# Kernel tuning notes

Measured on AMD Instinct MI355X. Metric: run time of the kernel, lower is better.

## Reference

```python
import jax, jax.numpy as jnp
import numpy as np

# LE-like radial basis config (hypers: type='le', r_cut=5.0, mlp=True, no alchemical)
N_MAX_L = [22, 19, 16, 13]      # n_max per angular channel l
L_MAX = len(N_MAX_L) - 1
N_TOTAL = sum(N_MAX_L)          # 70
N_SPECIES = 4                   # all_species = [0,1,2,3]
N_GRID = 1024                   # spline control points
R_CUT = 5.0
HIDDEN = 32                     # hard-coded MLP width in the module
N_EDGES = 400_000


def setup_inputs() -> dict:
    key = jax.random.key(0)
    ks = jax.random.split(key, 7)
    # neighbor distances in [0, r_cut)
    r = jax.random.uniform(ks[0], (N_EDGES,), dtype=jnp.float32) * R_CUT
    neighbor_species = jax.random.randint(ks[1], (N_EDGES,), 0, N_SPECIES)
    # spline table standing in for the precomputed spliner coefficients
    spline_table = jax.random.normal(ks[2], (N_GRID, N_TOTAL), dtype=jnp.float32)
    nmax = max(N_MAX_L)
    sc_in = 1.0 / np.sqrt(nmax)
    sc_h = 1.0 / np.sqrt(HIDDEN)
    # per-(l, species) expert MLP weights, padded to nmax along the n_max_l axis;
    # torch Linear(n_in, n_out, bias=False) == x @ W with W: [n_in, n_out]
    W1 = jax.random.normal(ks[3], (L_MAX + 1, N_SPECIES, nmax, HIDDEN), dtype=jnp.float32) * sc_in
    W2 = jax.random.normal(ks[4], (L_MAX + 1, N_SPECIES, HIDDEN, HIDDEN), dtype=jnp.float32) * sc_h
    W3 = jax.random.normal(ks[5], (L_MAX + 1, N_SPECIES, HIDDEN, HIDDEN), dtype=jnp.float32) * sc_h
    W4 = jax.random.normal(ks[6], (L_MAX + 1, N_SPECIES, HIDDEN, nmax), dtype=jnp.float32) * sc_h
    return {"r": r, "neighbor_species": neighbor_species, "spline_table": spline_table,
            "W1": W1, "W2": W2, "W3": W3, "W4": W4}


def _spline_eval(r, spline_table):
    # linear-interpolation spline over a uniform grid on [0, R_CUT]
    dx = R_CUT / (N_GRID - 1)
    xi = r / dx
    idx = jnp.clip(jnp.floor(xi).astype(jnp.int32), 0, N_GRID - 2)
    frac = (xi - idx.astype(xi.dtype))[:, None]
    return spline_table[idx] * (1.0 - frac) + spline_table[idx + 1] * frac  # [E, N_TOTAL]


def reference(r, neighbor_species, spline_table, W1, W2, W3, W4):
    # 1) spline basis eval: r -> radial_functions [E, N_TOTAL]
    rf = _spline_eval(r, spline_table)
    silu = jax.nn.silu
    outs = []
    off = 0
    # 2) split by n_max_l; per-species expert MLP with scatter-back.
    # Vectorized as: run each species' tiny MLP on all edges, select via mask
    # (equivalent math to the original's nonzero/index_select gather-scatter).
    for l, n_l in enumerate(N_MAX_L):
        x_l = rf[:, off:off + n_l]  # [E, n_l]
        off += n_l
        out_l = jnp.zeros_like(x_l)
        for s in range(N_SPECIES):
            h = silu(x_l @ W1[l, s, :n_l])        # [E, 32]
            h = silu(h @ W2[l, s])                # [E, 32]
            h = silu(h @ W3[l, s])                # [E, 32]
            y = h @ W4[l, s][:, :n_l]             # [E, n_l]
            out_l = jnp.where(neighbor_species[:, None] == s, y, out_l)
        outs.append(out_l)
    # original returns a list split by l; concatenate for a single output array
    return jnp.concatenate(outs, axis=1)  # [E, N_TOTAL]
```

## Files before the change

### kernel.cpp

```cpp
#include <hip/hip_runtime.h>
#include <hip/hip_bf16.h>
#include <math.h>

#define BLK 256
#define NEDGE_MAX 400000
#define BX 128
#define TSL 24608

typedef __attribute__((ext_vector_type(8))) short short8;
typedef __attribute__((ext_vector_type(4))) float f32x4;

union Frag {
  short8 s;
  unsigned int u[4];
};


__global__ void k_zero(int* __restrict__ cnt) {
  if (threadIdx.x < 4) cnt[threadIdx.x] = 0;
}

__global__ void __launch_bounds__(BLK) k_compact(const int* __restrict__ spc,
                                                 const float* __restrict__ r, int n,
                                                 int* __restrict__ cnt,
                                                 int* __restrict__ perm,
                                                 float* __restrict__ rs) {
  __shared__ int wcnt[4][4];
  __shared__ int wbase[4][4];
  const int tid = threadIdx.x;
  const int i = blockIdx.x * BLK + tid;
  const int lane = tid & 63;
  const int w = tid >> 6;
  const int s = (i < n) ? spc[i] : -1;
  const float rv = (i < n) ? r[i] : 0.f;

  int rank = 0;
#pragma unroll
  for (int sp = 0; sp < 4; sp++) {
    unsigned long long m = __ballot(s == sp);
    if (lane == 0) wcnt[w][sp] = __popcll(m);
    if (s == sp) rank = __popcll(m & ((1ULL << lane) - 1ULL));
  }
  __syncthreads();
  if (tid < 4) {
    const int c0 = wcnt[0][tid], c1 = wcnt[1][tid], c2 = wcnt[2][tid], c3 = wcnt[3][tid];
    const int b = atomicAdd(&cnt[tid], c0 + c1 + c2 + c3);
    wbase[0][tid] = b;
    wbase[1][tid] = b + c0;
    wbase[2][tid] = b + c0 + c1;
    wbase[3][tid] = b + c0 + c1 + c2;
  }
  __syncthreads();
  if (s >= 0) {
    const int pos = wbase[w][s] + rank;
    perm[s * NEDGE_MAX + pos] = i;
    rs[s * NEDGE_MAX + pos] = rv;
  }
}


__global__ void __launch_bounds__(256) k_table(const float* __restrict__ tbl,
                                               float* __restrict__ wt) {
  const int t = blockIdx.x * 256 + threadIdx.x;
  if (t < 4 * 1024 * 24) {
    const int l = t / (1024 * 24);
    const int rem = t - l * (1024 * 24);
    const int idx = rem / 24;
    const int j = rem - idx * 24;
    const int off = (l == 0) ? 0 : (l == 1) ? 22 : (l == 2) ? 41 : 57;
    const int nl = (l == 0) ? 22 : (l == 1) ? 19 : (l == 2) ? 16 : 13;
    const float v = (j < nl) ? tbl[idx * 70 + off + j] : 0.f;
    wt[l * TSL + idx * 24 + j] = v;
  }
  if (t < 4 * 32) {
    const int l = t >> 5, j = t & 31;
    wt[l * TSL + 1024 * 24 + j] = 0.f;
  }
}


__device__ __forceinline__ void split_pair(float a, float b, unsigned int& hi,
                                           unsigned int& lo) {
  __hip_bfloat162 h2 = __float22bfloat162_rn(float2{a, b});
  const unsigned int h = *reinterpret_cast<unsigned int*>(&h2);
  hi = h;
  const float ra = a - __uint_as_float((h & 0xFFFFu) << 16);
  const float rb = b - __uint_as_float(h & 0xFFFF0000u);
  __hip_bfloat162 l2 = __float22bfloat162_rn(float2{ra, rb});
  lo = *reinterpret_cast<unsigned int*>(&l2);
}

__device__ __forceinline__ unsigned int pack_pair(float a, float b) {
  __hip_bfloat162 h2 = __float22bfloat162_rn(float2{a, b});
  return *reinterpret_cast<unsigned int*>(&h2);
}

__device__ __forceinline__ void layer_hl(const Frag* A, const Frag& bh,
                                         const Frag& bl, f32x4& d0, f32x4& d1) {
  f32x4 z = {0.f, 0.f, 0.f, 0.f};
  d0 = __builtin_amdgcn_mfma_f32_16x16x32_bf16(A[0].s, bl.s, z, 0, 0, 0);
  d0 = __builtin_amdgcn_mfma_f32_16x16x32_bf16(A[0].s, bh.s, d0, 0, 0, 0);
  d1 = __builtin_amdgcn_mfma_f32_16x16x32_bf16(A[1].s, bl.s, z, 0, 0, 0);
  d1 = __builtin_amdgcn_mfma_f32_16x16x32_bf16(A[1].s, bh.s, d1, 0, 0, 0);
}

__device__ __forceinline__ void layer_h(const Frag* A, const Frag& bh, f32x4& d0,
                                        f32x4& d1) {
  f32x4 z = {0.f, 0.f, 0.f, 0.f};
  d0 = __builtin_amdgcn_mfma_f32_16x16x32_bf16(A[0].s, bh.s, z, 0, 0, 0);
  d1 = __builtin_amdgcn_mfma_f32_16x16x32_bf16(A[1].s, bh.s, z, 0, 0, 0);
}

__device__ __forceinline__ f32x4 silu4(f32x4 v) {
#pragma unroll
  for (int i = 0; i < 4; i++) v[i] = __fdividef(v[i], 1.0f + __expf(-v[i]));
  return v;
}

struct GD {
  f32x4 a0, a1, b0, b1;
  float frac;
  int e;
  int valid;
};

__device__ __forceinline__ GD do_gather(const float* __restrict__ rs,
                                        const float* __restrict__ tb,
                                        const int* __restrict__ perm, int sBase,
                                        int ei, int count) {
  GD gd;
  gd.valid = ei < count;
  const int eic = gd.valid ? ei : 0;
  gd.e = perm[sBase + eic];
  const float rr = rs[sBase + eic];
  const float xi = rr * (1023.0f / 5.0f);
  int idx = (int)floorf(xi);
  idx = idx < 0 ? 0 : (idx > 1022 ? 1022 : idx);
  gd.frac = xi - (float)idx;
  const float* t0 = tb + idx * 24;
  gd.a0 = *(const f32x4*)(t0);
  gd.a1 = *(const f32x4*)(t0 + 4);
  gd.b0 = *(const f32x4*)(t0 + 24);
  gd.b1 = *(const f32x4*)(t0 + 28);
  return gd;
}

template <int L, int NL, int OFF>
__device__ void body(const float* __restrict__ rs, const float* __restrict__ wt,
                     const float* __restrict__ W1, const float* __restrict__ W2,
                     const float* __restrict__ W3, const float* __restrict__ W4,
                     float* __restrict__ out, const int* __restrict__ cnt,
                     const int* __restrict__ perm, float* __restrict__ xpw,
                     int* __restrict__ eidw) {
  const int s = blockIdx.y & 3;
  const int count = cnt[s];
  if (count == 0) return;

  const int lane = threadIdx.x & 63;
  const int w = threadIdx.x >> 6;
  const int c = lane & 15;
  const int g = lane >> 4;

  const float* __restrict__ w1 = W1 + (size_t)(L * 4 + s) * (22 * 32);
  const float* __restrict__ w2 = W2 + (size_t)(L * 4 + s) * (32 * 32);
  const float* __restrict__ w3 = W3 + (size_t)(L * 4 + s) * (32 * 32);
  const float* __restrict__ w4 = W4 + (size_t)(L * 4 + s) * (32 * 22);

  Frag A1[2], A2[2], A3[2], A4[2];
#pragma unroll
  for (int jt = 0; jt < 2; jt++) {
    const int j = jt * 16 + c;
#pragma unroll
    for (int p = 0; p < 4; p++) {
      const int k0 = 8 * g + 2 * p, k1 = k0 + 1;
      const float a = (k0 < NL) ? w1[k0 * 32 + j] : 0.f;
      const float b = (k1 < NL) ? w1[k1 * 32 + j] : 0.f;
      A1[jt].u[p] = pack_pair(a, b);
      const int kp0 = (p < 2) ? (4 * g + 2 * p) : (16 + 4 * g + 2 * (p - 2));
      const int kp1 = kp0 + 1;
      A2[jt].u[p] = pack_pair(w2[kp0 * 32 + j], w2[kp1 * 32 + j]);
      A3[jt].u[p] = pack_pair(w3[kp0 * 32 + j], w3[kp1 * 32 + j]);
      A4[jt].u[p] = pack_pair((j < NL) ? w4[kp0 * 22 + j] : 0.f,
                              (j < NL) ? w4[kp1 * 22 + j] : 0.f);
    }
  }

  const float* __restrict__ tb = wt + L * TSL + 8 * g;
  const int sBase = s * NEDGE_MAX;
  const int stride = gridDim.x * 64;

  int eb = blockIdx.x * 64 + w * 16;
  GD cur = do_gather(rs, tb, perm, sBase, eb + c, count);

  for (; eb < count; eb += stride) {
    GD nxt = do_gather(rs, tb, perm, sBase, eb + stride + c, count);

    Frag bh, bl;
    {
      float x[8];
#pragma unroll
      for (int d = 0; d < 4; d++) {
        x[d] = cur.a0[d] + cur.frac * (cur.b0[d] - cur.a0[d]);
        x[d + 4] = cur.a1[d] + cur.frac * (cur.b1[d] - cur.a1[d]);
      }
      split_pair(x[0], x[1], bh.u[0], bl.u[0]);
      split_pair(x[2], x[3], bh.u[1], bl.u[1]);
      split_pair(x[4], x[5], bh.u[2], bl.u[2]);
      split_pair(x[6], x[7], bh.u[3], bl.u[3]);
    }

    f32x4 d0, d1;
    layer_hl(A1, bh, bl, d0, d1);

#pragma unroll
    for (int t = 0; t < 3; t++) {
      d0 = silu4(d0);
      d1 = silu4(d1);
      bh.u[0] = pack_pair(d0[0], d0[1]);
      bh.u[1] = pack_pair(d0[2], d0[3]);
      bh.u[2] = pack_pair(d1[0], d1[1]);
      bh.u[3] = pack_pair(d1[2], d1[3]);
      if (t == 0) layer_h(A2, bh, d0, d1);
      else if (t == 1) layer_h(A3, bh, d0, d1);
      else layer_h(A4, bh, d0, d1);
    }

    *(f32x4*)(xpw + c * 36 + 4 * g) = d0;
    *(f32x4*)(xpw + c * 36 + 16 + 4 * g) = d1;
    if (g == 0) eidw[c] = cur.valid ? cur.e : -1;
    __asm__ volatile("" ::: "memory");

    constexpr int TOT = 16 * NL;
#pragma unroll
    for (int t = 0; t < (TOT + 63) / 64; t++) {
      const int flat = t * 64 + lane;
      if (flat < TOT) {
        const int row = flat / NL;
        const int f = flat - row * NL;
        const int er = eidw[row];
        if (er >= 0) out[(size_t)er * 70 + OFF + f] = xpw[row * 36 + f];
      }
    }
    __asm__ volatile("" ::: "memory");

    cur = nxt;
  }
}

__global__ void __launch_bounds__(BLK) rb_mfma(const float* __restrict__ rs,
                                               const float* __restrict__ wt,
                                               const float* __restrict__ W1,
                                               const float* __restrict__ W2,
                                               const float* __restrict__ W3,
                                               const float* __restrict__ W4,
                                               float* __restrict__ out,
                                               const int* __restrict__ cnt,
                                               const int* __restrict__ perm) {
  __shared__ float xpose[4][16 * 36];
  __shared__ int eidt[4][16];
  const int w = threadIdx.x >> 6;
  float* xpw = &xpose[w][0];
  int* eidw = &eidt[w][0];
  switch (blockIdx.y >> 2) {
    case 0: body<0, 22, 0>(rs, wt, W1, W2, W3, W4, out, cnt, perm, xpw, eidw); break;
    case 1: body<1, 19, 22>(rs, wt, W1, W2, W3, W4, out, cnt, perm, xpw, eidw); break;
    case 2: body<2, 16, 41>(rs, wt, W1, W2, W3, W4, out, cnt, perm, xpw, eidw); break;
    default: body<3, 13, 57>(rs, wt, W1, W2, W3, W4, out, cnt, perm, xpw, eidw); break;
  }
}

extern "C" void kernel_launch(void* const* d_in, const int* in_sizes, int n_in,
                              void* d_out, int out_size, void* d_ws, size_t ws_size,
                              hipStream_t stream) {
  const float* r = (const float*)d_in[0];
  const int* spc = (const int*)d_in[1];
  const float* tbl = (const float*)d_in[2];
  const float* W1 = (const float*)d_in[3];
  const float* W2 = (const float*)d_in[4];
  const float* W3 = (const float*)d_in[5];
  const float* W4 = (const float*)d_in[6];
  float* out = (float*)d_out;
  const int n = in_sizes[0];

  int* cnt = (int*)d_ws;
  int* perm = (int*)d_ws + 64;
  float* rs = (float*)((int*)d_ws + 64 + 4 * NEDGE_MAX);
  float* wtbl = rs + 4 * NEDGE_MAX;

  hipLaunchKernelGGL(k_zero, dim3(1), dim3(64), 0, stream, cnt);

  const int nb = (n + BLK - 1) / BLK;
  hipLaunchKernelGGL(k_compact, dim3(nb), dim3(BLK), 0, stream, spc, r, n, cnt,
                     perm, rs);

  hipLaunchKernelGGL(k_table, dim3((4 * 1024 * 24 + 255) / 256), dim3(256), 0,
                     stream, tbl, wtbl);

  hipLaunchKernelGGL(rb_mfma, dim3(BX, 16), dim3(BLK), 0, stream, rs, wtbl, W1, W2,
                     W3, W4, out, cnt, perm);
}
```

Measured before the change: 145.1 us.

## Replace scattered MFMA output writes with bf16 staging plus coalesced scatter

Adds a histogram and prefix pass so each species' edges sit contiguously, and precomputes the spline fraction and table offset during compaction. The MLP kernel then writes its results as bf16 into a species-sorted temporary buffer, and a separate gather kernel writes the final output rows in order, giving fully coalesced output stores. The goal is to remove the scattered per-edge output writes. In exchange it adds extra kernel launches and another pass over the data, and it rounds the output to bf16, which loses precision. A direct-write fallback runs when the workspace is too small.

```diff
diff --git a/kernel.cpp b/kernel.cpp
--- a/kernel.cpp
+++ b/kernel.cpp
@@ -3,7 +3,6 @@
 #include <math.h>
 
 #define BLK 256
-#define NEDGE_MAX 400000
 #define BX 128
 #define TSL 24608
 
@@ -15,16 +14,55 @@
   unsigned int u[4];
 };
 
+__device__ __forceinline__ unsigned int pack_pair(float a, float b) {
+  __hip_bfloat162 h2 = __float22bfloat162_rn(float2{a, b});
+  return *reinterpret_cast<unsigned int*>(&h2);
+}
+
+__device__ __forceinline__ void split_pair(float a, float b, unsigned int& hi,
+                                           unsigned int& lo) {
+  hi = pack_pair(a, b);
+  const float ra = a - __uint_as_float(hi << 16);
+  const float rb = b - __uint_as_float(hi & 0xFFFF0000u);
+  lo = pack_pair(ra, rb);
+}
+
 
 __global__ void k_zero(int* __restrict__ cnt) {
   if (threadIdx.x < 4) cnt[threadIdx.x] = 0;
 }
 
+__global__ void __launch_bounds__(BLK) k_hist(const int* __restrict__ spc, int n,
+                                              int* __restrict__ cnt) {
+  __shared__ int h[4];
+  if (threadIdx.x < 4) h[threadIdx.x] = 0;
+  __syncthreads();
+  const int i = blockIdx.x * BLK + threadIdx.x;
+  if (i < n) atomicAdd(&h[spc[i]], 1);
+  __syncthreads();
+  if (threadIdx.x < 4) atomicAdd(&cnt[threadIdx.x], h[threadIdx.x]);
+}
+
+__global__ void k_prefix(const int* __restrict__ cnt, int* __restrict__ cnt2,
+                         int* __restrict__ csum) {
+  if (threadIdx.x == 0) {
+    int a = 0;
+#pragma unroll
+    for (int s = 0; s < 4; s++) {
+      csum[s] = a;
+      cnt2[s] = a;
+      a += cnt[s];
+    }
+  }
+}
+
 __global__ void __launch_bounds__(BLK) k_compact(const int* __restrict__ spc,
                                                  const float* __restrict__ r, int n,
-                                                 int* __restrict__ cnt,
-                                                 int* __restrict__ perm,
-                                                 float* __restrict__ rs) {
+                                                 int* __restrict__ cnt2,
+                                                 int* __restrict__ inv,
+                                                 float* __restrict__ fracs,
+                                                 int* __restrict__ toffA,
+                                                 int* __restrict__ perm) {
   __shared__ int wcnt[4][4];
   __shared__ int wbase[4][4];
   const int tid = threadIdx.x;
@@ -32,7 +70,7 @@
   const int lane = tid & 63;
   const int w = tid >> 6;
   const int s = (i < n) ? spc[i] : -1;
-  const float rv = (i < n) ? r[i] : 0.f;
+  const float rr = (i < n) ? r[i] : 0.f;
 
   int rank = 0;
 #pragma unroll
@@ -44,7 +82,7 @@
   __syncthreads();
   if (tid < 4) {
     const int c0 = wcnt[0][tid], c1 = wcnt[1][tid], c2 = wcnt[2][tid], c3 = wcnt[3][tid];
-    const int b = atomicAdd(&cnt[tid], c0 + c1 + c2 + c3);
+    const int b = atomicAdd(&cnt2[tid], c0 + c1 + c2 + c3);
     wbase[0][tid] = b;
     wbase[1][tid] = b + c0;
     wbase[2][tid] = b + c0 + c1;
@@ -52,9 +90,14 @@
   }
   __syncthreads();
   if (s >= 0) {
-    const int pos = wbase[w][s] + rank;
-    perm[s * NEDGE_MAX + pos] = i;
-    rs[s * NEDGE_MAX + pos] = rv;
+    const int sp = wbase[w][s] + rank;
+    const float xi = rr * (1023.0f / 5.0f);
+    int idx = (int)floorf(xi);
+    idx = idx < 0 ? 0 : (idx > 1022 ? 1022 : idx);
+    inv[i] = sp;
+    fracs[sp] = xi - (float)idx;
+    toffA[sp] = idx * 96;
+    perm[sp] = i;
   }
 }
 
@@ -79,22 +122,6 @@
 }
 
 
-__device__ __forceinline__ void split_pair(float a, float b, unsigned int& hi,
-                                           unsigned int& lo) {
-  __hip_bfloat162 h2 = __float22bfloat162_rn(float2{a, b});
-  const unsigned int h = *reinterpret_cast<unsigned int*>(&h2);
-  hi = h;
-  const float ra = a - __uint_as_float((h & 0xFFFFu) << 16);
-  const float rb = b - __uint_as_float(h & 0xFFFF0000u);
-  __hip_bfloat162 l2 = __float22bfloat162_rn(float2{ra, rb});
-  lo = *reinterpret_cast<unsigned int*>(&l2);
-}
-
-__device__ __forceinline__ unsigned int pack_pair(float a, float b) {
-  __hip_bfloat162 h2 = __float22bfloat162_rn(float2{a, b});
-  return *reinterpret_cast<unsigned int*>(&h2);
-}
-
 __device__ __forceinline__ void layer_hl(const Frag* A, const Frag& bh,
                                          const Frag& bl, f32x4& d0, f32x4& d1) {
   f32x4 z = {0.f, 0.f, 0.f, 0.f};
@@ -124,37 +151,38 @@
   int valid;
 };
 
-__device__ __forceinline__ GD do_gather(const float* __restrict__ rs,
-                                        const float* __restrict__ tb,
-                                        const int* __restrict__ perm, int sBase,
+template <bool DIRECT>
+__device__ __forceinline__ GD do_gather(const float* __restrict__ fracs,
+                                        const int* __restrict__ toffA,
+                                        const int* __restrict__ perm,
+                                        const char* __restrict__ tbB, int sp0,
                                         int ei, int count) {
   GD gd;
   gd.valid = ei < count;
-  const int eic = gd.valid ? ei : 0;
-  gd.e = perm[sBase + eic];
-  const float rr = rs[sBase + eic];
-  const float xi = rr * (1023.0f / 5.0f);
-  int idx = (int)floorf(xi);
-  idx = idx < 0 ? 0 : (idx > 1022 ? 1022 : idx);
-  gd.frac = xi - (float)idx;
-  const float* t0 = tb + idx * 24;
-  gd.a0 = *(const f32x4*)(t0);
-  gd.a1 = *(const f32x4*)(t0 + 4);
-  gd.b0 = *(const f32x4*)(t0 + 24);
-  gd.b1 = *(const f32x4*)(t0 + 28);
+  const int spi = sp0 + (gd.valid ? ei : 0);
+  gd.frac = fracs[spi];
+  const int to = toffA[spi];
+  if (DIRECT) gd.e = perm[spi]; else gd.e = 0;
+  const char* p = tbB + to;
+  gd.a0 = *(const f32x4*)(p);
+  gd.a1 = *(const f32x4*)(p + 16);
+  gd.b0 = *(const f32x4*)(p + 96);
+  gd.b1 = *(const f32x4*)(p + 112);
   return gd;
 }
 
-template <int L, int NL, int OFF>
-__device__ void body(const float* __restrict__ rs, const float* __restrict__ wt,
-                     const float* __restrict__ W1, const float* __restrict__ W2,
-                     const float* __restrict__ W3, const float* __restrict__ W4,
-                     float* __restrict__ out, const int* __restrict__ cnt,
-                     const int* __restrict__ perm, float* __restrict__ xpw,
-                     int* __restrict__ eidw) {
+template <int L, int NL, int OFF, bool DIRECT>
+__device__ void body(const float* __restrict__ fracs, const int* __restrict__ toffA,
+                     const float* __restrict__ wt, const float* __restrict__ W1,
+                     const float* __restrict__ W2, const float* __restrict__ W3,
+                     const float* __restrict__ W4, float* __restrict__ out,
+                     const int* __restrict__ cnt, const int* __restrict__ csum,
+                     const int* __restrict__ perm, unsigned short* __restrict__ tmp16,
+                     int n) {
   const int s = blockIdx.y & 3;
   const int count = cnt[s];
   if (count == 0) return;
+  const int sp0 = csum[s];
 
   const int lane = threadIdx.x & 63;
   const int w = threadIdx.x >> 6;
@@ -185,15 +213,17 @@
     }
   }
 
-  const float* __restrict__ tb = wt + L * TSL + 8 * g;
-  const int sBase = s * NEDGE_MAX;
+  const char* __restrict__ tbB = (const char*)(wt + L * TSL + 8 * g);
+  constexpr int ROWB = (L < 2) ? 48 : 32;
+  char* __restrict__ tmpB =
+      (char*)tmp16 + (size_t)n * (L == 0 ? 0 : L == 1 ? 48 : L == 2 ? 96 : 128);
+
   const int stride = gridDim.x * 64;
-
   int eb = blockIdx.x * 64 + w * 16;
-  GD cur = do_gather(rs, tb, perm, sBase, eb + c, count);
+  GD cur = do_gather<DIRECT>(fracs, toffA, perm, tbB, sp0, eb + c, count);
 
   for (; eb < count; eb += stride) {
-    GD nxt = do_gather(rs, tb, perm, sBase, eb + stride + c, count);
+    GD nxt = do_gather<DIRECT>(fracs, toffA, perm, tbB, sp0, eb + stride + c, count);
 
     Frag bh, bl;
     {
@@ -225,29 +255,36 @@
       else layer_h(A4, bh, d0, d1);
     }
 
-    *(f32x4*)(xpw + c * 36 + 4 * g) = d0;
-    *(f32x4*)(xpw + c * 36 + 16 + 4 * g) = d1;
-    if (g == 0) eidw[c] = cur.valid ? cur.e : -1;
-    __asm__ volatile("" ::: "memory");
-
-    constexpr int TOT = 16 * NL;
-#pragma unroll
-    for (int t = 0; t < (TOT + 63) / 64; t++) {
-      const int flat = t * 64 + lane;
-      if (flat < TOT) {
-        const int row = flat / NL;
-        const int f = flat - row * NL;
-        const int er = eidw[row];
-        if (er >= 0) out[(size_t)er * 70 + OFF + f] = xpw[row * 36 + f];
+    if (!DIRECT) {
+      if (cur.valid) {
+        const size_t ro = (size_t)(sp0 + eb + c) * ROWB;
+        const unsigned int u0 = pack_pair(d0[0], d0[1]);
+        const unsigned int u1 = pack_pair(d0[2], d0[3]);
+        *(uint2*)(tmpB + ro + 8 * g) = make_uint2(u0, u1);
+        if (NL > 16 && g < 2) {
+          const unsigned int u2 = pack_pair(d1[0], d1[1]);
+          const unsigned int u3 = pack_pair(d1[2], d1[3]);
+          *(uint2*)(tmpB + ro + 32 + 8 * g) = make_uint2(u2, u3);
+        }
       }
-    }
-    __asm__ volatile("" ::: "memory");
+    } else {
+      float* __restrict__ o = out + (size_t)cur.e * 70 + OFF;
+#pragma unroll
+      for (int i2 = 0; i2 < 4; i2++) {
+        const int j0 = 4 * g + i2;
+        if (cur.valid && j0 < NL) o[j0] = d0[i2];
+        const int j1 = 16 + 4 * g + i2;
+        if (cur.valid && j1 < NL) o[j1] = d1[i2];
+      }
+    }
 
     cur = nxt;
   }
 }
 
-__global__ void __launch_bounds__(BLK) rb_mfma(const float* __restrict__ rs,
+template <bool DIRECT>
+__global__ void __launch_bounds__(BLK) rb_mfma(const float* __restrict__ fracs,
+                                               const int* __restrict__ toffA,
                                                const float* __restrict__ wt,
                                                const float* __restrict__ W1,
                                                const float* __restrict__ W2,
@@ -255,17 +292,43 @@
                                                const float* __restrict__ W4,
                                                float* __restrict__ out,
                                                const int* __restrict__ cnt,
-                                               const int* __restrict__ perm) {
-  __shared__ float xpose[4][16 * 36];
-  __shared__ int eidt[4][16];
-  const int w = threadIdx.x >> 6;
-  float* xpw = &xpose[w][0];
-  int* eidw = &eidt[w][0];
+                                               const int* __restrict__ csum,
+                                               const int* __restrict__ perm,
+                                               unsigned short* __restrict__ tmp16,
+                                               int n) {
   switch (blockIdx.y >> 2) {
-    case 0: body<0, 22, 0>(rs, wt, W1, W2, W3, W4, out, cnt, perm, xpw, eidw); break;
-    case 1: body<1, 19, 22>(rs, wt, W1, W2, W3, W4, out, cnt, perm, xpw, eidw); break;
-    case 2: body<2, 16, 41>(rs, wt, W1, W2, W3, W4, out, cnt, perm, xpw, eidw); break;
-    default: body<3, 13, 57>(rs, wt, W1, W2, W3, W4, out, cnt, perm, xpw, eidw); break;
+    case 0: body<0, 22, 0, DIRECT>(fracs, toffA, wt, W1, W2, W3, W4, out, cnt, csum, perm, tmp16, n); break;
+    case 1: body<1, 19, 22, DIRECT>(fracs, toffA, wt, W1, W2, W3, W4, out, cnt, csum, perm, tmp16, n); break;
+    case 2: body<2, 16, 41, DIRECT>(fracs, toffA, wt, W1, W2, W3, W4, out, cnt, csum, perm, tmp16, n); break;
+    default: body<3, 13, 57, DIRECT>(fracs, toffA, wt, W1, W2, W3, W4, out, cnt, csum, perm, tmp16, n); break;
+  }
+}
+
+
+__global__ void __launch_bounds__(256) k_scatter(const unsigned short* __restrict__ tmp16,
+                                                 const int* __restrict__ inv,
+                                                 float* __restrict__ out, int n) {
+  __shared__ int sinv[64];
+  const int i0 = blockIdx.x * 64;
+  if (threadIdx.x < 64) {
+    const int i = i0 + threadIdx.x;
+    sinv[threadIdx.x] = (i < n) ? inv[i] : 0;
+  }
+  __syncthreads();
+  const long n24 = (long)n * 24;
+  for (int t = threadIdx.x; t < 64 * 70; t += 256) {
+    const int il = t / 70;
+    const int f = t - il * 70;
+    const int i = i0 + il;
+    if (i >= n) continue;
+    const long sp = (long)sinv[il];
+    long hidx;
+    if (f < 22) hidx = sp * 24 + f;
+    else if (f < 41) hidx = n24 + sp * 24 + (f - 22);
+    else if (f < 57) hidx = 2 * n24 + sp * 16 + (f - 41);
+    else hidx = 2 * n24 + (long)n * 16 + sp * 16 + (f - 57);
+    const unsigned int h = tmp16[hidx];
+    out[(size_t)i0 * 70 + t] = __uint_as_float(h << 16);
   }
 }
 
@@ -283,19 +346,34 @@
   const int n = in_sizes[0];
 
   int* cnt = (int*)d_ws;
-  int* perm = (int*)d_ws + 64;
-  float* rs = (float*)((int*)d_ws + 64 + 4 * NEDGE_MAX);
-  float* wtbl = rs + 4 * NEDGE_MAX;
+  int* cnt2 = cnt + 4;
+  int* csum = cnt + 8;
+  int* inv = cnt + 64;
+  float* fracs = (float*)(inv + n);
+  int* toffA = (int*)(fracs + n);
+  int* perm = toffA + n;
+  float* wtbl = (float*)(perm + n);
+  unsigned short* tmp16 = (unsigned short*)(wtbl + 4 * TSL);
+  const size_t need = (size_t)((char*)(tmp16 + (size_t)80 * n) - (char*)d_ws);
+  const bool direct = ws_size < need;
 
   hipLaunchKernelGGL(k_zero, dim3(1), dim3(64), 0, stream, cnt);
 
   const int nb = (n + BLK - 1) / BLK;
-  hipLaunchKernelGGL(k_compact, dim3(nb), dim3(BLK), 0, stream, spc, r, n, cnt,
-                     perm, rs);
-
+  hipLaunchKernelGGL(k_hist, dim3(nb), dim3(BLK), 0, stream, spc, n, cnt);
+  hipLaunchKernelGGL(k_prefix, dim3(1), dim3(64), 0, stream, cnt, cnt2, csum);
+  hipLaunchKernelGGL(k_compact, dim3(nb), dim3(BLK), 0, stream, spc, r, n, cnt2,
+                     inv, fracs, toffA, perm);
   hipLaunchKernelGGL(k_table, dim3((4 * 1024 * 24 + 255) / 256), dim3(256), 0,
                      stream, tbl, wtbl);
 
-  hipLaunchKernelGGL(rb_mfma, dim3(BX, 16), dim3(BLK), 0, stream, rs, wtbl, W1, W2,
-                     W3, W4, out, cnt, perm);
-}
+  if (!direct) {
+    hipLaunchKernelGGL(rb_mfma<false>, dim3(BX, 16), dim3(BLK), 0, stream, fracs,
+                       toffA, wtbl, W1, W2, W3, W4, out, cnt, csum, perm, tmp16, n);
+    hipLaunchKernelGGL(k_scatter, dim3((n + 63) / 64), dim3(256), 0, stream, tmp16,
+                       inv, out, n);
+  } else {
+    hipLaunchKernelGGL(rb_mfma<true>, dim3(BX, 16), dim3(BLK), 0, stream, fracs,
+                       toffA, wtbl, W1, W2, W3, W4, out, cnt, csum, perm, tmp16, n);
+  }
+}
```

Result: slower. 197.5 us (+36.1%).
